# Kernel optimization log

Measured on AMD Instinct MI355X. Metric: run time of the kernel, lower is better.

Reference implementation:

```python
import jax, jax.numpy as jnp
import numpy as np

VOCAB = 32000
HIDDEN = 512
B, T = 8, 512
LN_EPS = 1e-5


def setup_inputs() -> dict:
    key = jax.random.key(0)
    ks = jax.random.split(key, 9)
    s = 0.02
    return {
        "input_ids": jax.random.randint(ks[0], (B, T), 0, VOCAB),
        "emb": jax.random.normal(ks[1], (VOCAB, HIDDEN), jnp.float32) * s,
        "w_ih": jax.random.normal(ks[2], (3 * HIDDEN, HIDDEN), jnp.float32) * s,
        "w_hh": jax.random.normal(ks[3], (3 * HIDDEN, HIDDEN), jnp.float32) * s,
        "b_ih": jnp.zeros((3 * HIDDEN,), jnp.float32),
        "b_hh": jnp.zeros((3 * HIDDEN,), jnp.float32),
        "ln_gamma": jnp.ones((HIDDEN,), jnp.float32),
        "ln_beta": jnp.zeros((HIDDEN,), jnp.float32),
        "head_w": jax.random.normal(ks[4], (VOCAB, HIDDEN), jnp.float32) * s,
        "head_b": jnp.zeros((VOCAB,), jnp.float32),
    }


def _gru_scan(xg, w_hh, b_hh):
    # xg: [T, B, 3H]  (input-side gate pre-activations, PyTorch gate order r,z,n)
    H = xg.shape[-1] // 3
    h0 = jnp.zeros((xg.shape[1], H), xg.dtype)

    def step(h, xg_t):
        hg = h @ w_hh.T + b_hh              # [B, 3H]
        xr, xz, xn = jnp.split(xg_t, 3, axis=-1)
        hr, hz, hn = jnp.split(hg, 3, axis=-1)
        r = jax.nn.sigmoid(xr + hr)
        z = jax.nn.sigmoid(xz + hz)
        n = jnp.tanh(xn + r * hn)
        h_new = (1.0 - z) * n + z * h
        return h_new, h_new

    _, hs = jax.lax.scan(step, h0, xg)
    return hs  # [T, B, H]


def reference(input_ids, emb, w_ih, w_hh, b_ih, b_hh, ln_gamma, ln_beta, head_w, head_b):
    # embedding lookup: [B, T, H]
    x = emb[input_ids]
    # precompute input-side gate pre-activations for all timesteps: [B, T, 3H]
    xg = jnp.einsum("bth,gh->btg", x, w_ih) + b_ih
    # sequential GRU over time
    hs = _gru_scan(jnp.swapaxes(xg, 0, 1), w_hh, b_hh)  # [T, B, H]
    hs = jnp.swapaxes(hs, 0, 1)                          # [B, T, H]
    # LayerNorm over hidden dim
    mu = jnp.mean(hs, axis=-1, keepdims=True)
    var = jnp.mean(jnp.square(hs - mu), axis=-1, keepdims=True)
    y = (hs - mu) * jax.lax.rsqrt(var + LN_EPS) * ln_gamma + ln_beta
    # output head: [B, T, V]
    logits = jnp.einsum("bth,vh->btv", y, head_w) + head_b
    return logits
```

## Files before the change

kernel.cpp:

```cpp
#include <hip/hip_runtime.h>
#include <hip/hip_bf16.h>
#include <stdint.h>

#define VOCAB 32000
#define HID 512
#define NB 8
#define SEQ 512
#define NG 1536
#define LN_EPS 1e-5f
#define GRU_WGS 32
#define NWORK 224
#define TW 16
#define NTW (SEQ / TW)
#define NBN (VOCAB / 128)
#define GRU_SPIN_BUDGET (1 << 20)
#define WRK_SPIN_BUDGET (1 << 22)

typedef short bf16x8 __attribute__((ext_vector_type(8)));
typedef float f32x4 __attribute__((ext_vector_type(4)));

__device__ __forceinline__ unsigned short f2bf(float f) {
  union { float f; uint32_t u; } c; c.f = f;
  return (unsigned short)((c.u + 0x7fffu + ((c.u >> 16) & 1u)) >> 16);
}

__global__ void init_ws_kernel(unsigned short* h_state, int* flags) {
  int i = blockIdx.x * 256 + threadIdx.x;
  if (i < 2 * 16 * HID) h_state[i] = 0;
  if (i < GRU_WGS * 16) flags[i] = 0;
}

__global__ void conv_bf16_kernel(const float* __restrict__ in,
                                 unsigned short* __restrict__ out, int n4) {
  int i = blockIdx.x * 256 + threadIdx.x;
  if (i >= n4) return;
  const float4 v = ((const float4*)in)[i];
  ushort4 o;
  o.x = f2bf(v.x); o.y = f2bf(v.y); o.z = f2bf(v.z); o.w = f2bf(v.w);
  ((ushort4*)out)[i] = o;
}

__global__ void embed_kernel(const int* __restrict__ ids,
                             const float* __restrict__ emb,
                             unsigned short* __restrict__ out) {
  int row = blockIdx.x;
  int id = ids[row];
  int c = threadIdx.x * 2;
  const float2 v = *(const float2*)(emb + (size_t)id * HID + c);
  ushort2 o; o.x = f2bf(v.x); o.y = f2bf(v.y);
  *(ushort2*)(out + (size_t)row * HID + c) = o;
}

#define BM 128
#define BN 128
#define BK 32

__global__ __launch_bounds__(256, 2) void gemm_bt_kernel(
    const unsigned short* __restrict__ A, const unsigned short* __restrict__ B,
    const float* __restrict__ bias, float* __restrict__ C, int N, int nbn) {
  __shared__ unsigned short a_lds[BM * BK];
  __shared__ unsigned short b_lds[BN * BK];
  const int nwg = gridDim.x;
  const int chunk = nwg >> 3;
  const int bid = blockIdx.x;
  const int sw = (bid & 7) * chunk + (bid >> 3);
  const int bm = sw / nbn, bn = sw % nbn;
  const int tid = threadIdx.x;
  const int lane = tid & 63, wid = tid >> 6;
  const int wm = wid >> 1, wn = wid & 1;

  f32x4 acc[4][4] = {};

  for (int kt = 0; kt < HID / BK; ++kt) {
    __syncthreads();
#pragma unroll
    for (int p = 0; p < 2; ++p) {
      const int flat = (p * 256 + tid) * 16;
      const int row = flat >> 6;
      const int kb = flat & 63;
      const char* ga =
          (const char*)(A + ((size_t)(bm * BM + row) * HID + kt * BK)) + kb;
      const char* gb =
          (const char*)(B + ((size_t)(bn * BN + row) * HID + kt * BK)) + kb;
      char* la = (char*)a_lds + (size_t)(p * 256 + wid * 64) * 16;
      char* lb = (char*)b_lds + (size_t)(p * 256 + wid * 64) * 16;
      __builtin_amdgcn_global_load_lds(
          (const __attribute__((address_space(1))) void*)ga,
          (__attribute__((address_space(3))) void*)la, 16, 0, 0);
      __builtin_amdgcn_global_load_lds(
          (const __attribute__((address_space(1))) void*)gb,
          (__attribute__((address_space(3))) void*)lb, 16, 0, 0);
    }
    __syncthreads();
    bf16x8 af[4], bfr[4];
#pragma unroll
    for (int i = 0; i < 4; ++i) {
      af[i] = *(const bf16x8*)(a_lds + (wm * 64 + i * 16 + (lane & 15)) * BK +
                               (lane >> 4) * 8);
      bfr[i] = *(const bf16x8*)(b_lds + (wn * 64 + i * 16 + (lane & 15)) * BK +
                                (lane >> 4) * 8);
    }
#pragma unroll
    for (int i = 0; i < 4; ++i)
#pragma unroll
      for (int j = 0; j < 4; ++j)
        acc[i][j] =
            __builtin_amdgcn_mfma_f32_16x16x32_bf16(af[i], bfr[j], acc[i][j], 0, 0, 0);
  }
#pragma unroll
  for (int i = 0; i < 4; ++i) {
    const int mrow = bm * BM + wm * 64 + i * 16 + (lane >> 4) * 4;
#pragma unroll
    for (int j = 0; j < 4; ++j) {
      const int col = bn * BN + wn * 64 + j * 16 + (lane & 15);
      const float bv = bias[col];
#pragma unroll
      for (int r = 0; r < 4; ++r)
        C[(size_t)(mrow + r) * N + col] = acc[i][j][r] + bv;
    }
  }
}

__global__ __launch_bounds__(256, 1) void mega_kernel(
    const float* __restrict__ xg, const float* __restrict__ w_hh,
    const float* __restrict__ b_hh, float* __restrict__ hs,
    unsigned short* __restrict__ h_state, int* __restrict__ flags,
    const unsigned short* __restrict__ hwb, const float* __restrict__ head_b,
    const float* __restrict__ gamma, const float* __restrict__ beta,
    float* __restrict__ out) {
  __shared__ float h_pub[8][16];
  __shared__ unsigned short a_lds[128 * 32];
  __shared__ unsigned short b_lds[128 * 32];
  __shared__ float mu_lds[128];
  __shared__ float is_lds[128];

  const int tid = threadIdx.x;

  if (blockIdx.x < GRU_WGS) {
    if (tid >= 64) return;
    const int wid = blockIdx.x;
    const int lane = tid;
    const int col16 = lane & 15;
    const int kq = lane >> 4;

    bf16x8 wf[3][16];
#pragma unroll
    for (int g = 0; g < 3; ++g) {
      const float* wr =
          w_hh + (size_t)(g * HID + wid * 16 + col16) * HID + kq * 8;
#pragma unroll
      for (int kk = 0; kk < 16; ++kk) {
        float4 f0 = *(const float4*)(wr + kk * 32);
        float4 f1 = *(const float4*)(wr + kk * 32 + 4);
        bf16x8 v;
        v[0] = (short)f2bf(f0.x); v[1] = (short)f2bf(f0.y);
        v[2] = (short)f2bf(f0.z); v[3] = (short)f2bf(f0.w);
        v[4] = (short)f2bf(f1.x); v[5] = (short)f2bf(f1.y);
        v[6] = (short)f2bf(f1.z); v[7] = (short)f2bf(f1.w);
        wf[g][kk] = v;
      }
    }
    const float bh_r = b_hh[0 * HID + wid * 16 + col16];
    const float bh_z = b_hh[1 * HID + wid * 16 + col16];
    const float bh_n = b_hh[2 * HID + wid * 16 + col16];

    const int abase = col16 * HID + kq * 8;
    const bool realrow = col16 < 8;
    const bool owner = lane < 32;
    const int bbase = kq * 4;

    float xr[4], xz[4], xn[4];
#pragma unroll
    for (int r = 0; r < 4; ++r) { xr[r] = 0.f; xz[r] = 0.f; xn[r] = 0.f; }
    if (owner) {
#pragma unroll
      for (int r = 0; r < 4; ++r) {
        const size_t xo = (size_t)(bbase + r) * SEQ * NG + wid * 16 + col16;
        xr[r] = xg[xo];
        xz[r] = xg[xo + HID];
        xn[r] = xg[xo + 2 * HID];
      }
    }
    float hprev[4] = {0.f, 0.f, 0.f, 0.f};
    int budget = GRU_SPIN_BUDGET;

    for (int t = 0; t < SEQ; ++t) {
      while (budget > 0) {
        int v = t;
        if (lane < 32)
          v = __hip_atomic_load(flags + lane * 16, __ATOMIC_RELAXED,
                                __HIP_MEMORY_SCOPE_AGENT);
        if (__ballot(v >= t) == ~0ULL) break;
        --budget;
        __builtin_amdgcn_s_sleep(1);
      }

      const unsigned short* rd = h_state + (size_t)(t & 1) * (16 * HID);
      unsigned short* wpub = h_state + (size_t)((t + 1) & 1) * (16 * HID);

      uint64_t hb[32];
#pragma unroll
      for (int kk = 0; kk < 32; ++kk) hb[kk] = 0;
      if (realrow) {
#pragma unroll
        for (int kk = 0; kk < 16; ++kk) {
          const uint64_t* ap = (const uint64_t*)(rd + abase + kk * 32);
          hb[2 * kk] = __hip_atomic_load(ap, __ATOMIC_RELAXED,
                                         __HIP_MEMORY_SCOPE_AGENT);
          hb[2 * kk + 1] = __hip_atomic_load(ap + 1, __ATOMIC_RELAXED,
                                             __HIP_MEMORY_SCOPE_AGENT);
        }
      }

      f32x4 ar = {0.f, 0.f, 0.f, 0.f};
      f32x4 az = {0.f, 0.f, 0.f, 0.f};
      f32x4 an = {0.f, 0.f, 0.f, 0.f};
#pragma unroll
      for (int kk = 0; kk < 16; ++kk) {
        union { uint64_t u[2]; bf16x8 v; } cv;
        cv.u[0] = hb[2 * kk]; cv.u[1] = hb[2 * kk + 1];
        ar = __builtin_amdgcn_mfma_f32_16x16x32_bf16(cv.v, wf[0][kk], ar, 0, 0, 0);
        az = __builtin_amdgcn_mfma_f32_16x16x32_bf16(cv.v, wf[1][kk], az, 0, 0, 0);
        an = __builtin_amdgcn_mfma_f32_16x16x32_bf16(cv.v, wf[2][kk], an, 0, 0, 0);
      }

      if (owner) {
#pragma unroll
        for (int r = 0; r < 4; ++r) {
          const float rg = 1.f / (1.f + __expf(-(xr[r] + ar[r] + bh_r)));
          const float zg = 1.f / (1.f + __expf(-(xz[r] + az[r] + bh_z)));
          const float a = xn[r] + rg * (an[r] + bh_n);
          const float e2 = __expf(-2.f * fabsf(a));
          const float nn = copysignf((1.f - e2) / (1.f + e2), a);
          const float hnew = (1.f - zg) * nn + zg * hprev[r];
          hprev[r] = hnew;
          h_pub[bbase + r][col16] = hnew;
          union { float f; uint32_t u; } cv; cv.f = hnew;
          uint32_t* hp = (uint32_t*)(hs + ((size_t)(bbase + r) * SEQ + t) * HID +
                                     wid * 16 + col16);
          __hip_atomic_store(hp, cv.u, __ATOMIC_RELAXED,
                             __HIP_MEMORY_SCOPE_AGENT);
        }
      }
      asm volatile("s_waitcnt lgkmcnt(0)" ::: "memory");
      __builtin_amdgcn_sched_barrier(0);
      {
        const int tb = lane >> 3;
        const int tc = (lane & 7) * 2;
        const float2 hp = *(const float2*)&h_pub[tb][tc];
        union { unsigned short s[2]; uint32_t u; } pk;
        pk.s[0] = f2bf(hp.x);
        pk.s[1] = f2bf(hp.y);
        uint32_t* dst = (uint32_t*)(wpub + tb * HID + wid * 16 + tc);
        __hip_atomic_store(dst, pk.u, __ATOMIC_RELAXED,
                           __HIP_MEMORY_SCOPE_AGENT);
      }
      asm volatile("s_waitcnt vmcnt(0)" ::: "memory");
      if (lane == 0)
        __hip_atomic_store(flags + wid * 16, t + 1, __ATOMIC_RELAXED,
                           __HIP_MEMORY_SCOPE_AGENT);
      if (owner && t + 1 < SEQ) {
#pragma unroll
        for (int r = 0; r < 4; ++r) {
          const size_t xo = (size_t)(bbase + r) * SEQ * NG +
                            (size_t)(t + 1) * NG + wid * 16 + col16;
          xr[r] = xg[xo]; xz[r] = xg[xo + HID]; xn[r] = xg[xo + 2 * HID];
        }
      }
    }
    return;
  }

  const int w = blockIdx.x - GRU_WGS;
  const int lane = tid & 63, wv = tid >> 6;
  const int wm = wv >> 1, wn = wv & 1;

  for (int ti = w; ti < NTW * NBN; ti += NWORK) {
    const int twi = ti / NBN;
    const int bn = ti - twi * NBN;
    const int t0 = twi * TW;
    const int tneed = t0 + TW;

    if (tid < 64) {
      int bud = WRK_SPIN_BUDGET;
      while (bud-- > 0) {
        int v = 0x7fffffff;
        if (lane < 32)
          v = __hip_atomic_load(flags + lane * 16, __ATOMIC_RELAXED,
                                __HIP_MEMORY_SCOPE_AGENT);
        if (__ballot(v >= tneed) == ~0ULL) break;
        __builtin_amdgcn_s_sleep(8);
      }
    }
    __syncthreads();

    for (int rr = 0; rr < 32; ++rr) {
      const int i = wv * 32 + rr;
      const int grow = ((i >> 4) * SEQ) + t0 + (i & 15);
      const uint64_t* xp = (const uint64_t*)(hs + (size_t)grow * HID) + lane * 4;
      float s = 0.f, q = 0.f;
#pragma unroll
      for (int j = 0; j < 4; ++j) {
        union { uint64_t u; float f[2]; } cv;
        cv.u = __hip_atomic_load(xp + j, __ATOMIC_RELAXED,
                                 __HIP_MEMORY_SCOPE_AGENT);
        s += cv.f[0] + cv.f[1];
        q += cv.f[0] * cv.f[0] + cv.f[1] * cv.f[1];
      }
#pragma unroll
      for (int off = 32; off > 0; off >>= 1) {
        s += __shfl_xor(s, off);
        q += __shfl_xor(q, off);
      }
      if (lane == 0) {
        const float mu = s * (1.f / 512.f);
        mu_lds[i] = mu;
        is_lds[i] = rsqrtf(q * (1.f / 512.f) - mu * mu + LN_EPS);
      }
    }
    __syncthreads();

    f32x4 acc[4][4] = {};
    for (int kt = 0; kt < 16; ++kt) {
      __syncthreads();
#pragma unroll
      for (int p = 0; p < 2; ++p) {
        const int flat = (p * 256 + tid) * 16;
        const int row = flat >> 6;
        const int kb = flat & 63;
        const char* gb =
            (const char*)(hwb + ((size_t)(bn * 128 + row) * HID + kt * 32)) + kb;
        char* lb = (char*)b_lds + (size_t)(p * 256 + wv * 64) * 16;
        __builtin_amdgcn_global_load_lds(
            (const __attribute__((address_space(1))) void*)gb,
            (__attribute__((address_space(3))) void*)lb, 16, 0, 0);
      }
      {
        const int arow = tid >> 1, ah = (tid & 1) * 16;
        const int grow = ((arow >> 4) * SEQ) + t0 + (arow & 15);
        const uint64_t* ap =
            (const uint64_t*)(hs + (size_t)grow * HID + kt * 32 + ah);
        float av[16];
#pragma unroll
        for (int j = 0; j < 8; ++j) {
          union { uint64_t u; float f[2]; } cv;
          cv.u = __hip_atomic_load(ap + j, __ATOMIC_RELAXED,
                                   __HIP_MEMORY_SCOPE_AGENT);
          av[2 * j] = cv.f[0];
          av[2 * j + 1] = cv.f[1];
        }
        const float mu = mu_lds[arow], isv = is_lds[arow];
        const float* gp = gamma + kt * 32 + ah;
        const float* bp = beta + kt * 32 + ah;
        union { unsigned short s[16]; uint4 u[2]; } pk;
#pragma unroll
        for (int j = 0; j < 16; ++j)
          pk.s[j] = f2bf((av[j] - mu) * isv * gp[j] + bp[j]);
        uint4* ad = (uint4*)((char*)a_lds + arow * 64 + ah * 2);
        ad[0] = pk.u[0];
        ad[1] = pk.u[1];
      }
      __syncthreads();
      bf16x8 af[4], bfr[4];
#pragma unroll
      for (int i = 0; i < 4; ++i) {
        af[i] = *(const bf16x8*)(a_lds + (wm * 64 + i * 16 + (lane & 15)) * 32 +
                                 (lane >> 4) * 8);
        bfr[i] = *(const bf16x8*)(b_lds + (wn * 64 + i * 16 + (lane & 15)) * 32 +
                                  (lane >> 4) * 8);
      }
#pragma unroll
      for (int i = 0; i < 4; ++i)
#pragma unroll
        for (int j = 0; j < 4; ++j)
          acc[i][j] = __builtin_amdgcn_mfma_f32_16x16x32_bf16(af[i], bfr[j],
                                                              acc[i][j], 0, 0, 0);
    }
#pragma unroll
    for (int i = 0; i < 4; ++i) {
#pragma unroll
      for (int j = 0; j < 4; ++j) {
        const int col = bn * 128 + wn * 64 + j * 16 + (lane & 15);
        const float bv = head_b[col];
#pragma unroll
        for (int r = 0; r < 4; ++r) {
          const int mrowl = wm * 64 + i * 16 + (lane >> 4) * 4 + r;
          const int grow = ((mrowl >> 4) * SEQ) + t0 + (mrowl & 15);
          out[(size_t)grow * VOCAB + col] = acc[i][j][r] + bv;
        }
      }
    }
  }
}

extern "C" void kernel_launch(void* const* d_in, const int* in_sizes, int n_in,
                              void* d_out, int out_size, void* d_ws,
                              size_t ws_size, hipStream_t stream) {
  const int* ids = (const int*)d_in[0];
  const float* emb = (const float*)d_in[1];
  const float* w_ih = (const float*)d_in[2];
  const float* w_hh = (const float*)d_in[3];
  const float* b_ih = (const float*)d_in[4];
  const float* b_hh = (const float*)d_in[5];
  const float* gamma = (const float*)d_in[6];
  const float* beta = (const float*)d_in[7];
  const float* head_w = (const float*)d_in[8];
  const float* head_b = (const float*)d_in[9];
  float* out = (float*)d_out;

  char* ws = (char*)d_ws;
  size_t off = 0;
  auto alloc = [&](size_t bytes) -> void* {
    void* p = ws + off;
    off = (off + bytes + 255) & ~(size_t)255;
    return p;
  };
  int* flags = (int*)alloc(GRU_WGS * 16 * sizeof(int));
  unsigned short* h_state = (unsigned short*)alloc(2 * 16 * HID * 2);
  unsigned short* A1 = (unsigned short*)alloc((size_t)NB * SEQ * HID * 2);
  unsigned short* wihb = (unsigned short*)alloc((size_t)NG * HID * 2);
  unsigned short* hwb = (unsigned short*)alloc((size_t)VOCAB * HID * 2);
  float* xg = (float*)alloc((size_t)NB * SEQ * NG * 4);
  float* hsb = (float*)alloc((size_t)NB * SEQ * HID * 4);

  init_ws_kernel<<<64, 256, 0, stream>>>(h_state, flags);
  conv_bf16_kernel<<<(NG * HID / 4) / 256, 256, 0, stream>>>(w_ih, wihb,
                                                             NG * HID / 4);
  conv_bf16_kernel<<<(VOCAB * HID / 4) / 256, 256, 0, stream>>>(
      head_w, hwb, VOCAB * HID / 4);
  embed_kernel<<<NB * SEQ, 256, 0, stream>>>(ids, emb, A1);
  gemm_bt_kernel<<<(NB * SEQ / BM) * (NG / BN), 256, 0, stream>>>(
      A1, wihb, b_ih, xg, NG, NG / BN);
  mega_kernel<<<GRU_WGS + NWORK, 256, 0, stream>>>(
      xg, w_hh, b_hh, hsb, h_state, flags, hwb, head_b, gamma, beta, out);
}
```

Measured before the change: 1.957 ms.

## Precompute LayerNorm bf16 activations once per time window and restructure head GEMM tiles

Worker blocks first take one 16-step time window each. They wait on coarse per-window GRU flags, compute LayerNorm once, and write the normalized activations as bf16 to a workspace buffer, then set a window-ready flag. Head GEMM tiles then read that bf16 buffer directly instead of recomputing LN from fp32 hidden states for each of the 250 vocab tiles. Other changes: the tile becomes 32 rows x 128 columns per wave, output stores are nontemporal, and the GRU hidden-state stores move after the flag publish. In exchange it adds an extra global buffer and pass, plus the serialized LN work on the first worker blocks.

```diff
diff --git a/kernel.cpp b/kernel.cpp
--- a/kernel.cpp
+++ b/kernel.cpp
@@ -9,7 +9,7 @@
 #define NG 1536
 #define LN_EPS 1e-5f
 #define GRU_WGS 32
-#define NWORK 224
+#define NWRK 224
 #define TW 16
 #define NTW (SEQ / TW)
 #define NBN (VOCAB / 128)
@@ -24,10 +24,10 @@
   return (unsigned short)((c.u + 0x7fffu + ((c.u >> 16) & 1u)) >> 16);
 }
 
-__global__ void init_ws_kernel(unsigned short* h_state, int* flags) {
+__global__ void init_ws_kernel(int* ibase, unsigned short* h_state) {
   int i = blockIdx.x * 256 + threadIdx.x;
+  if (i < 1536) ibase[i] = 0;
   if (i < 2 * 16 * HID) h_state[i] = 0;
-  if (i < GRU_WGS * 16) flags[i] = 0;
 }
 
 __global__ void conv_bf16_kernel(const float* __restrict__ in,
@@ -124,15 +124,18 @@
 __global__ __launch_bounds__(256, 1) void mega_kernel(
     const float* __restrict__ xg, const float* __restrict__ w_hh,
     const float* __restrict__ b_hh, float* __restrict__ hs,
-    unsigned short* __restrict__ h_state, int* __restrict__ flags,
+    unsigned short* __restrict__ h_state, int* __restrict__ ibase,
     const unsigned short* __restrict__ hwb, const float* __restrict__ head_b,
     const float* __restrict__ gamma, const float* __restrict__ beta,
-    float* __restrict__ out) {
+    unsigned short* __restrict__ yb, float* __restrict__ out) {
+  int* flags = ibase;
+  int* gflags = ibase + 512;
+  int* wflag = ibase + 1024;
+
   __shared__ float h_pub[8][16];
-  __shared__ unsigned short a_lds[128 * 32];
   __shared__ unsigned short b_lds[128 * 32];
-  __shared__ float mu_lds[128];
-  __shared__ float is_lds[128];
+  __shared__ float st_s[256], st_q[256];
+  __shared__ float mu_lds[128], is_lds[128];
 
   const int tid = threadIdx.x;
 
@@ -224,6 +227,7 @@
         an = __builtin_amdgcn_mfma_f32_16x16x32_bf16(cv.v, wf[2][kk], an, 0, 0, 0);
       }
 
+      float hnew[4] = {0.f, 0.f, 0.f, 0.f};
       if (owner) {
 #pragma unroll
         for (int r = 0; r < 4; ++r) {
@@ -232,14 +236,9 @@
           const float a = xn[r] + rg * (an[r] + bh_n);
           const float e2 = __expf(-2.f * fabsf(a));
           const float nn = copysignf((1.f - e2) / (1.f + e2), a);
-          const float hnew = (1.f - zg) * nn + zg * hprev[r];
-          hprev[r] = hnew;
-          h_pub[bbase + r][col16] = hnew;
-          union { float f; uint32_t u; } cv; cv.f = hnew;
-          uint32_t* hp = (uint32_t*)(hs + ((size_t)(bbase + r) * SEQ + t) * HID +
-                                     wid * 16 + col16);
-          __hip_atomic_store(hp, cv.u, __ATOMIC_RELAXED,
-                             __HIP_MEMORY_SCOPE_AGENT);
+          hnew[r] = (1.f - zg) * nn + zg * hprev[r];
+          hprev[r] = hnew[r];
+          h_pub[bbase + r][col16] = hnew[r];
         }
       }
       asm volatile("s_waitcnt lgkmcnt(0)" ::: "memory");
@@ -256,137 +255,166 @@
                            __HIP_MEMORY_SCOPE_AGENT);
       }
       asm volatile("s_waitcnt vmcnt(0)" ::: "memory");
-      if (lane == 0)
+      if (lane == 0) {
         __hip_atomic_store(flags + wid * 16, t + 1, __ATOMIC_RELAXED,
                            __HIP_MEMORY_SCOPE_AGENT);
-      if (owner && t + 1 < SEQ) {
+        if ((t & (TW - 1)) == 0 && t > 0)
+          __hip_atomic_store(gflags + wid * 16, t, __ATOMIC_RELAXED,
+                             __HIP_MEMORY_SCOPE_AGENT);
+      }
+      if (owner) {
 #pragma unroll
         for (int r = 0; r < 4; ++r) {
-          const size_t xo = (size_t)(bbase + r) * SEQ * NG +
-                            (size_t)(t + 1) * NG + wid * 16 + col16;
-          xr[r] = xg[xo]; xz[r] = xg[xo + HID]; xn[r] = xg[xo + 2 * HID];
+          union { float f; uint32_t u; } cv; cv.f = hnew[r];
+          __hip_atomic_store(
+              (uint32_t*)(hs + ((size_t)(bbase + r) * SEQ + t) * HID +
+                          wid * 16 + col16),
+              cv.u, __ATOMIC_RELAXED, __HIP_MEMORY_SCOPE_AGENT);
         }
-      }
-    }
+        if (t + 1 < SEQ) {
+#pragma unroll
+          for (int r = 0; r < 4; ++r) {
+            const size_t xo = (size_t)(bbase + r) * SEQ * NG +
+                              (size_t)(t + 1) * NG + wid * 16 + col16;
+            xr[r] = xg[xo]; xz[r] = xg[xo + HID]; xn[r] = xg[xo + 2 * HID];
+          }
+        }
+      }
+    }
+    asm volatile("s_waitcnt vmcnt(0)" ::: "memory");
+    if (tid == 0)
+      __hip_atomic_store(gflags + wid * 16, SEQ, __ATOMIC_RELAXED,
+                         __HIP_MEMORY_SCOPE_AGENT);
     return;
   }
 
   const int w = blockIdx.x - GRU_WGS;
   const int lane = tid & 63, wv = tid >> 6;
-  const int wm = wv >> 1, wn = wv & 1;
-
-  for (int ti = w; ti < NTW * NBN; ti += NWORK) {
-    const int twi = ti / NBN;
-    const int bn = ti - twi * NBN;
-    const int t0 = twi * TW;
-    const int tneed = t0 + TW;
-
+
+  if (w < NTW) {
+    const int t0 = w * TW;
+    const int need = t0 + TW;
     if (tid < 64) {
       int bud = WRK_SPIN_BUDGET;
-      while (bud-- > 0) {
+      for (;;) {
         int v = 0x7fffffff;
         if (lane < 32)
-          v = __hip_atomic_load(flags + lane * 16, __ATOMIC_RELAXED,
+          v = __hip_atomic_load(gflags + lane * 16, __ATOMIC_RELAXED,
                                 __HIP_MEMORY_SCOPE_AGENT);
-        if (__ballot(v >= tneed) == ~0ULL) break;
+        if (__ballot(v >= need) == ~0ULL || --bud <= 0) break;
         __builtin_amdgcn_s_sleep(8);
       }
     }
     __syncthreads();
-
-    for (int rr = 0; rr < 32; ++rr) {
-      const int i = wv * 32 + rr;
-      const int grow = ((i >> 4) * SEQ) + t0 + (i & 15);
-      const uint64_t* xp = (const uint64_t*)(hs + (size_t)grow * HID) + lane * 4;
-      float s = 0.f, q = 0.f;
-#pragma unroll
-      for (int j = 0; j < 4; ++j) {
-        union { uint64_t u; float f[2]; } cv;
-        cv.u = __hip_atomic_load(xp + j, __ATOMIC_RELAXED,
+    const int row = tid >> 1, half = tid & 1;
+    const int grow = (row >> 4) * SEQ + t0 + (row & 15);
+    const uint64_t* hp = (const uint64_t*)(hs + (size_t)grow * HID) + half * 128;
+    float s = 0.f, q = 0.f;
+    for (int j = 0; j < 128; ++j) {
+      union { uint64_t u; float f[2]; } cv;
+      cv.u = __hip_atomic_load(hp + j, __ATOMIC_RELAXED,
+                               __HIP_MEMORY_SCOPE_AGENT);
+      s += cv.f[0] + cv.f[1];
+      q += cv.f[0] * cv.f[0] + cv.f[1] * cv.f[1];
+    }
+    st_s[tid] = s; st_q[tid] = q;
+    __syncthreads();
+    if (tid < 128) {
+      const float ss = st_s[2 * tid] + st_s[2 * tid + 1];
+      const float qq = st_q[2 * tid] + st_q[2 * tid + 1];
+      const float mu = ss * (1.f / 512.f);
+      mu_lds[tid] = mu;
+      is_lds[tid] = rsqrtf(qq * (1.f / 512.f) - mu * mu + LN_EPS);
+    }
+    __syncthreads();
+    {
+      const float mu = mu_lds[row], isv = is_lds[row];
+      unsigned short* yp = yb + (size_t)grow * HID + half * 256;
+      const float* gp = gamma + half * 256;
+      const float* bp = beta + half * 256;
+      for (int j = 0; j < 64; ++j) {
+        union { uint64_t u; float f[2]; } a0, a1;
+        a0.u = __hip_atomic_load(hp + 2 * j, __ATOMIC_RELAXED,
                                  __HIP_MEMORY_SCOPE_AGENT);
-        s += cv.f[0] + cv.f[1];
-        q += cv.f[0] * cv.f[0] + cv.f[1] * cv.f[1];
-      }
-#pragma unroll
-      for (int off = 32; off > 0; off >>= 1) {
-        s += __shfl_xor(s, off);
-        q += __shfl_xor(q, off);
-      }
-      if (lane == 0) {
-        const float mu = s * (1.f / 512.f);
-        mu_lds[i] = mu;
-        is_lds[i] = rsqrtf(q * (1.f / 512.f) - mu * mu + LN_EPS);
-      }
-    }
-    __syncthreads();
-
-    f32x4 acc[4][4] = {};
+        a1.u = __hip_atomic_load(hp + 2 * j + 1, __ATOMIC_RELAXED,
+                                 __HIP_MEMORY_SCOPE_AGENT);
+        union { unsigned short s4[4]; uint64_t u; } pk;
+        pk.s4[0] = f2bf((a0.f[0] - mu) * isv * gp[4 * j + 0] + bp[4 * j + 0]);
+        pk.s4[1] = f2bf((a0.f[1] - mu) * isv * gp[4 * j + 1] + bp[4 * j + 1]);
+        pk.s4[2] = f2bf((a1.f[0] - mu) * isv * gp[4 * j + 2] + bp[4 * j + 2]);
+        pk.s4[3] = f2bf((a1.f[1] - mu) * isv * gp[4 * j + 3] + bp[4 * j + 3]);
+        __hip_atomic_store((uint64_t*)(yp + 4 * j), pk.u, __ATOMIC_RELAXED,
+                           __HIP_MEMORY_SCOPE_AGENT);
+      }
+    }
+    asm volatile("s_waitcnt vmcnt(0)" ::: "memory");
+    __syncthreads();
+    if (tid == 0)
+      __hip_atomic_store(wflag + w * 16, 1, __ATOMIC_RELAXED,
+                         __HIP_MEMORY_SCOPE_AGENT);
+  }
+
+  for (int ti = w; ti < NTW * NBN; ti += NWRK) {
+    const int twi = ti / NBN, bn = ti - twi * NBN;
+    const int t0 = twi * TW;
+    if (tid == 0) {
+      int bud = WRK_SPIN_BUDGET;
+      while (__hip_atomic_load(wflag + twi * 16, __ATOMIC_RELAXED,
+                               __HIP_MEMORY_SCOPE_AGENT) == 0 &&
+             --bud > 0)
+        __builtin_amdgcn_s_sleep(16);
+    }
+    __syncthreads();
+
+    f32x4 acc[2][8] = {};
     for (int kt = 0; kt < 16; ++kt) {
       __syncthreads();
 #pragma unroll
       for (int p = 0; p < 2; ++p) {
         const int flat = (p * 256 + tid) * 16;
-        const int row = flat >> 6;
+        const int brow = flat >> 6;
         const int kb = flat & 63;
         const char* gb =
-            (const char*)(hwb + ((size_t)(bn * 128 + row) * HID + kt * 32)) + kb;
+            (const char*)(hwb + ((size_t)(bn * 128 + brow) * HID + kt * 32)) +
+            kb;
         char* lb = (char*)b_lds + (size_t)(p * 256 + wv * 64) * 16;
         __builtin_amdgcn_global_load_lds(
             (const __attribute__((address_space(1))) void*)gb,
             (__attribute__((address_space(3))) void*)lb, 16, 0, 0);
       }
-      {
-        const int arow = tid >> 1, ah = (tid & 1) * 16;
-        const int grow = ((arow >> 4) * SEQ) + t0 + (arow & 15);
-        const uint64_t* ap =
-            (const uint64_t*)(hs + (size_t)grow * HID + kt * 32 + ah);
-        float av[16];
-#pragma unroll
-        for (int j = 0; j < 8; ++j) {
-          union { uint64_t u; float f[2]; } cv;
-          cv.u = __hip_atomic_load(ap + j, __ATOMIC_RELAXED,
-                                   __HIP_MEMORY_SCOPE_AGENT);
-          av[2 * j] = cv.f[0];
-          av[2 * j + 1] = cv.f[1];
-        }
-        const float mu = mu_lds[arow], isv = is_lds[arow];
-        const float* gp = gamma + kt * 32 + ah;
-        const float* bp = beta + kt * 32 + ah;
-        union { unsigned short s[16]; uint4 u[2]; } pk;
-#pragma unroll
-        for (int j = 0; j < 16; ++j)
-          pk.s[j] = f2bf((av[j] - mu) * isv * gp[j] + bp[j]);
-        uint4* ad = (uint4*)((char*)a_lds + arow * 64 + ah * 2);
-        ad[0] = pk.u[0];
-        ad[1] = pk.u[1];
+      bf16x8 af[2];
+#pragma unroll
+      for (int i = 0; i < 2; ++i) {
+        const int row_l = wv * 32 + i * 16 + (lane & 15);
+        const int ga = (row_l >> 4) * SEQ + t0 + (row_l & 15);
+        af[i] = *(const bf16x8*)(yb + (size_t)ga * HID + kt * 32 +
+                                 (lane >> 4) * 8);
       }
       __syncthreads();
-      bf16x8 af[4], bfr[4];
-#pragma unroll
-      for (int i = 0; i < 4; ++i) {
-        af[i] = *(const bf16x8*)(a_lds + (wm * 64 + i * 16 + (lane & 15)) * 32 +
-                                 (lane >> 4) * 8);
-        bfr[i] = *(const bf16x8*)(b_lds + (wn * 64 + i * 16 + (lane & 15)) * 32 +
+      bf16x8 bfr[8];
+#pragma unroll
+      for (int j = 0; j < 8; ++j)
+        bfr[j] = *(const bf16x8*)(b_lds + (j * 16 + (lane & 15)) * 32 +
                                   (lane >> 4) * 8);
-      }
-#pragma unroll
-      for (int i = 0; i < 4; ++i)
-#pragma unroll
-        for (int j = 0; j < 4; ++j)
+#pragma unroll
+      for (int i = 0; i < 2; ++i)
+#pragma unroll
+        for (int j = 0; j < 8; ++j)
           acc[i][j] = __builtin_amdgcn_mfma_f32_16x16x32_bf16(af[i], bfr[j],
                                                               acc[i][j], 0, 0, 0);
     }
 #pragma unroll
-    for (int i = 0; i < 4; ++i) {
-#pragma unroll
-      for (int j = 0; j < 4; ++j) {
-        const int col = bn * 128 + wn * 64 + j * 16 + (lane & 15);
+    for (int i = 0; i < 2; ++i) {
+#pragma unroll
+      for (int j = 0; j < 8; ++j) {
+        const int col = bn * 128 + j * 16 + (lane & 15);
         const float bv = head_b[col];
 #pragma unroll
         for (int r = 0; r < 4; ++r) {
-          const int mrowl = wm * 64 + i * 16 + (lane >> 4) * 4 + r;
-          const int grow = ((mrowl >> 4) * SEQ) + t0 + (mrowl & 15);
-          out[(size_t)grow * VOCAB + col] = acc[i][j][r] + bv;
+          const int row_l = wv * 32 + i * 16 + (lane >> 4) * 4 + r;
+          const int ga = (row_l >> 4) * SEQ + t0 + (row_l & 15);
+          __builtin_nontemporal_store(acc[i][j][r] + bv,
+                                      &out[(size_t)ga * VOCAB + col]);
         }
       }
     }
@@ -415,15 +443,16 @@
     off = (off + bytes + 255) & ~(size_t)255;
     return p;
   };
-  int* flags = (int*)alloc(GRU_WGS * 16 * sizeof(int));
+  int* ibase = (int*)alloc(1536 * sizeof(int));
   unsigned short* h_state = (unsigned short*)alloc(2 * 16 * HID * 2);
   unsigned short* A1 = (unsigned short*)alloc((size_t)NB * SEQ * HID * 2);
   unsigned short* wihb = (unsigned short*)alloc((size_t)NG * HID * 2);
   unsigned short* hwb = (unsigned short*)alloc((size_t)VOCAB * HID * 2);
   float* xg = (float*)alloc((size_t)NB * SEQ * NG * 4);
   float* hsb = (float*)alloc((size_t)NB * SEQ * HID * 4);
-
-  init_ws_kernel<<<64, 256, 0, stream>>>(h_state, flags);
+  unsigned short* yb = (unsigned short*)alloc((size_t)NB * SEQ * HID * 2);
+
+  init_ws_kernel<<<64, 256, 0, stream>>>(ibase, h_state);
   conv_bf16_kernel<<<(NG * HID / 4) / 256, 256, 0, stream>>>(w_ih, wihb,
                                                              NG * HID / 4);
   conv_bf16_kernel<<<(VOCAB * HID / 4) / 256, 256, 0, stream>>>(
@@ -431,6 +460,6 @@
   embed_kernel<<<NB * SEQ, 256, 0, stream>>>(ids, emb, A1);
   gemm_bt_kernel<<<(NB * SEQ / BM) * (NG / BN), 256, 0, stream>>>(
       A1, wihb, b_ih, xg, NG, NG / BN);
-  mega_kernel<<<GRU_WGS + NWORK, 256, 0, stream>>>(
-      xg, w_hh, b_hh, hsb, h_state, flags, hwb, head_b, gamma, beta, out);
-}
+  mega_kernel<<<GRU_WGS + NWRK, 256, 0, stream>>>(
+      xg, w_hh, b_hh, hsb, h_state, ibase, hwb, head_b, gamma, beta, yb, out);
+}
```

New measurement: 2.043 ms. 1.04x slower.
